# Kernel tuning notes

Hardware: AMD Instinct MI355X
Metric: run time of the kernel (lower is better)

## Reference

```python
import jax, jax.numpy as jnp
import numpy as np

# Assumptions (helpers not included in source):
#  - drop_edge(A, 0.8, training) is identity at inference (training=False); we
#    implement the deterministic eval path.
#  - normalized_laplacian_tilde_matrix(A) = D~^{-1/2} (A + I) D~^{-1/2}, the
#    renormalization-trick adjacency (A_tilde = A + I, D~ = rowsum(A_tilde)).

def setup_inputs() -> dict:
    key = jax.random.key(0)
    kx, kA, kW = jax.random.split(key, 3)
    B, C, Co, T, N, K = 64, 64, 64, 32, 64, 3
    x = jax.random.normal(kx, (B, C, T, N), dtype=jnp.float32)
    A = jax.random.uniform(kA, (B, K, T, N, N), dtype=jnp.float32)
    W = jax.random.normal(kW, (Co, C), dtype=jnp.float32) * 0.02  # 1x1 conv weight
    b = jnp.zeros((Co,), dtype=jnp.float32)
    return {"x": x, "A": A, "W": W, "b": b}


def reference(x, A, W, b):
    # 1x1 Conv2d == per-position channel mixing
    x = jnp.einsum('bctn,oc->botn', x, W) + b[None, :, None, None]

    # Vectorized normalized-Laplacian-tilde over all (B, K, T) graphs at once.
    N = A.shape[-1]
    A_tilde = A + jnp.eye(N, dtype=A.dtype)            # (B,K,T,N,N)
    deg = jnp.sum(A_tilde, axis=-1)                    # (B,K,T,N)
    dinv = jax.lax.rsqrt(deg)                          # deg >= 1, safe
    A_norm = A_tilde * dinv[..., :, None] * dinv[..., None, :]

    # Per-(k,t) bmm: out[b,c,t,m] = sum_k sum_n x[b,c,t,n] * A_norm[b,k,t,n,m]
    x_out = jnp.einsum('bctn,bktnm->bctm', x, A_norm)
    return (x_out, A)
```

## Files before the change

kernel.cpp:

```cpp
#include <hip/hip_runtime.h>
#include <hip/hip_bf16.h>

typedef __attribute__((ext_vector_type(8))) short short8;
typedef __attribute__((ext_vector_type(4))) short short4v;
typedef __attribute__((ext_vector_type(4))) float f32x4;

#define Bb 64
#define Cc 64
#define Tt 32
#define Nn 64
#define Kk 3
#define PITCH 72
#define OUT_A_OFF 8388608L

__device__ __forceinline__ short f2bf(float f) {
    __hip_bfloat16 h = __float2bfloat16(f);
    return *reinterpret_cast<short*>(&h);
}

__global__ __launch_bounds__(256, 4) void ctg_kernel(
    const float* __restrict__ X,
    const float* __restrict__ A,
    const float* __restrict__ W,
    const float* __restrict__ bias,
    float* __restrict__ out)
{
    __shared__ short sW [Cc * PITCH];
    __shared__ short sXT[Nn * PITCH];
    __shared__ short sX1[Cc * PITCH];
    __shared__ short sAT[Nn * PITCH];
    __shared__ float sDinv[Nn];
    __shared__ float sB[Cc];

    const int tid = threadIdx.x;
    const int b = blockIdx.x >> 5;
    const int t = blockIdx.x & 31;
    const int l  = tid & 63;
    const int w  = tid >> 6;
    const int lr = l & 15;
    const int lq = l >> 4;

    const long xbase = (long)b * (Cc * Tt * Nn) + (long)t * Nn;

    #pragma unroll
    for (int j = 0; j < 4; ++j) {
        int q  = tid + 256 * j;
        int r  = q >> 4;
        int c0 = (q & 15) * 4;
        f32x4 wv = *(const f32x4*)(W + r * 64 + c0);
        short4v ws;
        #pragma unroll
        for (int i = 0; i < 4; ++i) ws[i] = f2bf(wv[i]);
        *(short4v*)&sW[r * PITCH + c0] = ws;
        f32x4 xv = *(const f32x4*)(X + xbase + (long)r * (Tt * Nn) + c0);
        #pragma unroll
        for (int i = 0; i < 4; ++i) sXT[(c0 + i) * PITCH + r] = f2bf(xv[i]);
    }
    if (tid < Cc) sB[tid] = bias[tid];
    __syncthreads();

    short8 aw0 = *(const short8*)&sW[(16 * w + lr) * PITCH + 8 * lq];
    short8 aw1 = *(const short8*)&sW[(16 * w + lr) * PITCH + 32 + 8 * lq];
    f32x4 acc1[4];
    #pragma unroll
    for (int nt = 0; nt < 4; ++nt) {
        acc1[nt] = (f32x4){0.f, 0.f, 0.f, 0.f};
        short8 b0 = *(const short8*)&sXT[(16 * nt + lr) * PITCH + 8 * lq];
        short8 b1 = *(const short8*)&sXT[(16 * nt + lr) * PITCH + 32 + 8 * lq];
        acc1[nt] = __builtin_amdgcn_mfma_f32_16x16x32_bf16(aw0, b0, acc1[nt], 0, 0, 0);
        acc1[nt] = __builtin_amdgcn_mfma_f32_16x16x32_bf16(aw1, b1, acc1[nt], 0, 0, 0);
    }
    #pragma unroll
    for (int nt = 0; nt < 4; ++nt)
        #pragma unroll
        for (int r = 0; r < 4; ++r) {
            int c = 16 * w + 4 * lq + r;
            sX1[c * PITCH + 16 * nt + lr] = f2bf(acc1[nt][r] + sB[c]);
        }

    f32x4 acc3[4];
    #pragma unroll
    for (int mt = 0; mt < 4; ++mt) acc3[mt] = (f32x4){0.f, 0.f, 0.f, 0.f};

    const int m0 = (tid & 15) * 4;
    const long Abase0 = (long)b * (Kk * Tt * Nn * Nn) + (long)t * (Nn * Nn);

    for (int k = 0; k < Kk; ++k) {
        __syncthreads();

        const long Ab = Abase0 + (long)k * (Tt * Nn * Nn);
        f32x4 av[4];
        #pragma unroll
        for (int e = 0; e < 4; ++e) av[e] = *(const f32x4*)(A + Ab + 4 * (tid + 256 * e));
        #pragma unroll
        for (int e = 0; e < 4; ++e) *(f32x4*)(out + OUT_A_OFF + Ab + 4 * (tid + 256 * e)) = av[e];

        float dg[4];
        #pragma unroll
        for (int e = 0; e < 4; ++e) {
            float q = av[e][0] + av[e][1] + av[e][2] + av[e][3];
            q += __shfl_xor(q, 1);
            q += __shfl_xor(q, 2);
            q += __shfl_xor(q, 4);
            q += __shfl_xor(q, 8);
            dg[e] = q;
        }
        if ((tid & 15) == 0) {
            #pragma unroll
            for (int e = 0; e < 4; ++e)
                sDinv[(tid >> 4) + 16 * e] = rsqrtf(dg[e] + 1.0f);
        }
        __syncthreads();

        float dm[4] = { sDinv[m0], sDinv[m0 + 1], sDinv[m0 + 2], sDinv[m0 + 3] };
        #pragma unroll
        for (int e = 0; e < 4; ++e) {
            int n = (tid >> 4) + 16 * e;
            float dn = sDinv[n];
            #pragma unroll
            for (int i = 0; i < 4; ++i) {
                float v = av[e][i];
                if (m0 + i == n) v += 1.0f;
                sAT[(m0 + i) * PITCH + n] = f2bf(v * dn * dm[i]);
            }
        }
        __syncthreads();

        short8 a0 = *(const short8*)&sX1[(16 * w + lr) * PITCH + 8 * lq];
        short8 a1 = *(const short8*)&sX1[(16 * w + lr) * PITCH + 32 + 8 * lq];
        #pragma unroll
        for (int mt = 0; mt < 4; ++mt) {
            short8 b0 = *(const short8*)&sAT[(16 * mt + lr) * PITCH + 8 * lq];
            short8 b1 = *(const short8*)&sAT[(16 * mt + lr) * PITCH + 32 + 8 * lq];
            acc3[mt] = __builtin_amdgcn_mfma_f32_16x16x32_bf16(a0, b0, acc3[mt], 0, 0, 0);
            acc3[mt] = __builtin_amdgcn_mfma_f32_16x16x32_bf16(a1, b1, acc3[mt], 0, 0, 0);
        }
    }

    #pragma unroll
    for (int mt = 0; mt < 4; ++mt)
        #pragma unroll
        for (int r = 0; r < 4; ++r) {
            int c = 16 * w + 4 * lq + r;
            out[xbase + (long)c * (Tt * Nn) + 16 * mt + lr] = acc3[mt][r];
        }
}

extern "C" void kernel_launch(void* const* d_in, const int* in_sizes, int n_in,
                              void* d_out, int out_size, void* d_ws, size_t ws_size,
                              hipStream_t stream) {
    const float* X    = (const float*)d_in[0];
    const float* A    = (const float*)d_in[1];
    const float* W    = (const float*)d_in[2];
    const float* bias = (const float*)d_in[3];
    float* out = (float*)d_out;
    ctg_kernel<<<dim3(Bb * Tt), dim3(256), 0, stream>>>(X, A, W, bias, out);
}
```

Measured before the change: 243.6 us.

## Sum normalized adjacency over K in registers before a single MFMA pass

The kernel now builds the normalized adjacency for each k in registers and sums it over K in fp32. It then writes the summed matrix to shared memory once and runs one MFMA pass, instead of staging and multiplying per k. This removes two block barriers per k and two-thirds of the shared-memory staging and MFMA work for the graph product. It also adds an XOR-swizzled 64-wide shared layout and loads W and bias directly into registers. Occupancy is raised via launch bounds (256, 8), and outputs use nontemporal stores. The costs are more live registers for the 4x4 accumulators and different rounding, since the bf16 conversion now happens after the K-sum.

```diff
diff --git a/kernel.cpp b/kernel.cpp
--- a/kernel.cpp
+++ b/kernel.cpp
@@ -2,7 +2,6 @@
 #include <hip/hip_bf16.h>
 
 typedef __attribute__((ext_vector_type(8))) short short8;
-typedef __attribute__((ext_vector_type(4))) short short4v;
 typedef __attribute__((ext_vector_type(4))) float f32x4;
 
 #define Bb 64
@@ -18,55 +17,67 @@
     return *reinterpret_cast<short*>(&h);
 }
 
-__global__ __launch_bounds__(256, 4) void ctg_kernel(
+#define SWZ(row) ((((row) >> 3) ^ (row)) & 7)
+#define SADDR(row, col) (((row) << 6) + ((col) ^ (SWZ(row) << 3)))
+
+__global__ __launch_bounds__(256, 8) void ctg_kernel(
     const float* __restrict__ X,
     const float* __restrict__ A,
     const float* __restrict__ W,
     const float* __restrict__ bias,
     float* __restrict__ out)
 {
-    __shared__ short sW [Cc * PITCH];
-    __shared__ short sXT[Nn * PITCH];
-    __shared__ short sX1[Cc * PITCH];
-    __shared__ short sAT[Nn * PITCH];
-    __shared__ float sDinv[Nn];
-    __shared__ float sB[Cc];
+    __shared__ __attribute__((aligned(16))) short sU [64 * 64];
+    __shared__ __attribute__((aligned(16))) short sX1[Cc * PITCH];
+    __shared__ __attribute__((aligned(16))) float sDv[Kk][Nn];
 
-    const int tid = threadIdx.x;
-    const int b = blockIdx.x >> 5;
-    const int t = blockIdx.x & 31;
-    const int l  = tid & 63;
-    const int w  = tid >> 6;
-    const int lr = l & 15;
-    const int lq = l >> 4;
+    const int tid  = threadIdx.x;
+    const int b    = blockIdx.x >> 5;
+    const int t    = blockIdx.x & 31;
+    const int l    = tid & 63;
+    const int w    = tid >> 6;
+    const int lr   = l & 15;
+    const int lq   = l >> 4;
+    const int m0   = 4 * (tid & 15);
+    const int nrow = tid >> 4;
 
-    const long xbase = (long)b * (Cc * Tt * Nn) + (long)t * Nn;
+    const long xbase  = (long)b * (Cc * Tt * Nn) + (long)t * Nn;
+    const long Abase0 = (long)b * (Kk * Tt * Nn * Nn) + (long)t * (Nn * Nn);
 
     #pragma unroll
     for (int j = 0; j < 4; ++j) {
-        int q  = tid + 256 * j;
-        int r  = q >> 4;
-        int c0 = (q & 15) * 4;
-        f32x4 wv = *(const f32x4*)(W + r * 64 + c0);
-        short4v ws;
+        int c  = nrow + 16 * j;
+        f32x4 xv = *(const f32x4*)(X + xbase + (long)c * (Tt * Nn) + m0);
         #pragma unroll
-        for (int i = 0; i < 4; ++i) ws[i] = f2bf(wv[i]);
-        *(short4v*)&sW[r * PITCH + c0] = ws;
-        f32x4 xv = *(const f32x4*)(X + xbase + (long)r * (Tt * Nn) + c0);
-        #pragma unroll
-        for (int i = 0; i < 4; ++i) sXT[(c0 + i) * PITCH + r] = f2bf(xv[i]);
+        for (int i = 0; i < 4; ++i)
+            sU[SADDR(m0 + i, c)] = f2bf(xv[i]);
     }
-    if (tid < Cc) sB[tid] = bias[tid];
+
+    const float* wrow = W + (16 * w + lr) * Cc;
+    f32x4 wv0 = *(const f32x4*)(wrow + 8 * lq);
+    f32x4 wv1 = *(const f32x4*)(wrow + 8 * lq + 4);
+    f32x4 wv2 = *(const f32x4*)(wrow + 32 + 8 * lq);
+    f32x4 wv3 = *(const f32x4*)(wrow + 32 + 8 * lq + 4);
+    f32x4 bv  = *(const f32x4*)(bias + 16 * w + 4 * lq);
+    short8 aw0, aw1;
+    #pragma unroll
+    for (int i = 0; i < 4; ++i) {
+        aw0[i]     = f2bf(wv0[i]);
+        aw0[i + 4] = f2bf(wv1[i]);
+        aw1[i]     = f2bf(wv2[i]);
+        aw1[i + 4] = f2bf(wv3[i]);
+    }
+
     __syncthreads();
 
-    short8 aw0 = *(const short8*)&sW[(16 * w + lr) * PITCH + 8 * lq];
-    short8 aw1 = *(const short8*)&sW[(16 * w + lr) * PITCH + 32 + 8 * lq];
     f32x4 acc1[4];
     #pragma unroll
     for (int nt = 0; nt < 4; ++nt) {
+        const int row = 16 * nt + lr;
+        const int sw  = SWZ(row);
+        short8 b0 = *(const short8*)&sU[(row << 6) + ((lq ^ sw) << 3)];
+        short8 b1 = *(const short8*)&sU[(row << 6) + (((4 + lq) ^ sw) << 3)];
         acc1[nt] = (f32x4){0.f, 0.f, 0.f, 0.f};
-        short8 b0 = *(const short8*)&sXT[(16 * nt + lr) * PITCH + 8 * lq];
-        short8 b1 = *(const short8*)&sXT[(16 * nt + lr) * PITCH + 32 + 8 * lq];
         acc1[nt] = __builtin_amdgcn_mfma_f32_16x16x32_bf16(aw0, b0, acc1[nt], 0, 0, 0);
         acc1[nt] = __builtin_amdgcn_mfma_f32_16x16x32_bf16(aw1, b1, acc1[nt], 0, 0, 0);
     }
@@ -75,27 +86,26 @@
         #pragma unroll
         for (int r = 0; r < 4; ++r) {
             int c = 16 * w + 4 * lq + r;
-            sX1[c * PITCH + 16 * nt + lr] = f2bf(acc1[nt][r] + sB[c]);
+            sX1[c * PITCH + 16 * nt + lr] = f2bf(acc1[nt][r] + bv[r]);
         }
 
-    f32x4 acc3[4];
+    float S[4][4];
     #pragma unroll
-    for (int mt = 0; mt < 4; ++mt) acc3[mt] = (f32x4){0.f, 0.f, 0.f, 0.f};
-
-    const int m0 = (tid & 15) * 4;
-    const long Abase0 = (long)b * (Kk * Tt * Nn * Nn) + (long)t * (Nn * Nn);
+    for (int e = 0; e < 4; ++e)
+        #pragma unroll
+        for (int i = 0; i < 4; ++i) S[e][i] = 0.f;
 
     for (int k = 0; k < Kk; ++k) {
-        __syncthreads();
-
         const long Ab = Abase0 + (long)k * (Tt * Nn * Nn);
         f32x4 av[4];
         #pragma unroll
-        for (int e = 0; e < 4; ++e) av[e] = *(const f32x4*)(A + Ab + 4 * (tid + 256 * e));
+        for (int e = 0; e < 4; ++e)
+            av[e] = *(const f32x4*)(A + Ab + 4 * (tid + 256 * e));
         #pragma unroll
-        for (int e = 0; e < 4; ++e) *(f32x4*)(out + OUT_A_OFF + Ab + 4 * (tid + 256 * e)) = av[e];
+        for (int e = 0; e < 4; ++e)
+            __builtin_nontemporal_store(av[e], (f32x4*)(out + OUT_A_OFF + Ab + 4 * (tid + 256 * e)));
 
-        float dg[4];
+        float dnv[4];
         #pragma unroll
         for (int e = 0; e < 4; ++e) {
             float q = av[e][0] + av[e][1] + av[e][2] + av[e][3];
@@ -103,38 +113,49 @@
             q += __shfl_xor(q, 2);
             q += __shfl_xor(q, 4);
             q += __shfl_xor(q, 8);
-            dg[e] = q;
+            dnv[e] = rsqrtf(q + 1.0f);
         }
         if ((tid & 15) == 0) {
             #pragma unroll
-            for (int e = 0; e < 4; ++e)
-                sDinv[(tid >> 4) + 16 * e] = rsqrtf(dg[e] + 1.0f);
+            for (int e = 0; e < 4; ++e) sDv[k][nrow + 16 * e] = dnv[e];
         }
         __syncthreads();
 
-        float dm[4] = { sDinv[m0], sDinv[m0 + 1], sDinv[m0 + 2], sDinv[m0 + 3] };
+        f32x4 dm = *(const f32x4*)&sDv[k][m0];
         #pragma unroll
         for (int e = 0; e < 4; ++e) {
-            int n = (tid >> 4) + 16 * e;
-            float dn = sDinv[n];
+            const int n  = nrow + 16 * e;
+            const float dn = dnv[e];
             #pragma unroll
             for (int i = 0; i < 4; ++i) {
                 float v = av[e][i];
                 if (m0 + i == n) v += 1.0f;
-                sAT[(m0 + i) * PITCH + n] = f2bf(v * dn * dm[i]);
+                S[e][i] += v * dn * dm[i];
             }
         }
-        __syncthreads();
+    }
 
-        short8 a0 = *(const short8*)&sX1[(16 * w + lr) * PITCH + 8 * lq];
-        short8 a1 = *(const short8*)&sX1[(16 * w + lr) * PITCH + 32 + 8 * lq];
+    #pragma unroll
+    for (int e = 0; e < 4; ++e) {
+        int n = nrow + 16 * e;
         #pragma unroll
-        for (int mt = 0; mt < 4; ++mt) {
-            short8 b0 = *(const short8*)&sAT[(16 * mt + lr) * PITCH + 8 * lq];
-            short8 b1 = *(const short8*)&sAT[(16 * mt + lr) * PITCH + 32 + 8 * lq];
-            acc3[mt] = __builtin_amdgcn_mfma_f32_16x16x32_bf16(a0, b0, acc3[mt], 0, 0, 0);
-            acc3[mt] = __builtin_amdgcn_mfma_f32_16x16x32_bf16(a1, b1, acc3[mt], 0, 0, 0);
-        }
+        for (int i = 0; i < 4; ++i)
+            sU[SADDR(m0 + i, n)] = f2bf(S[e][i]);
+    }
+    __syncthreads();
+
+    const short8 a0 = *(const short8*)&sX1[(16 * w + lr) * PITCH + 8 * lq];
+    const short8 a1 = *(const short8*)&sX1[(16 * w + lr) * PITCH + 32 + 8 * lq];
+    f32x4 acc3[4];
+    #pragma unroll
+    for (int mt = 0; mt < 4; ++mt) {
+        const int row = 16 * mt + lr;
+        const int sw  = SWZ(row);
+        short8 b0 = *(const short8*)&sU[(row << 6) + ((lq ^ sw) << 3)];
+        short8 b1 = *(const short8*)&sU[(row << 6) + (((4 + lq) ^ sw) << 3)];
+        acc3[mt] = (f32x4){0.f, 0.f, 0.f, 0.f};
+        acc3[mt] = __builtin_amdgcn_mfma_f32_16x16x32_bf16(a0, b0, acc3[mt], 0, 0, 0);
+        acc3[mt] = __builtin_amdgcn_mfma_f32_16x16x32_bf16(a1, b1, acc3[mt], 0, 0, 0);
     }
 
     #pragma unroll
@@ -142,7 +163,8 @@
         #pragma unroll
         for (int r = 0; r < 4; ++r) {
             int c = 16 * w + 4 * lq + r;
-            out[xbase + (long)c * (Tt * Nn) + 16 * mt + lr] = acc3[mt][r];
+            __builtin_nontemporal_store(acc3[mt][r],
+                out + xbase + (long)c * (Tt * Nn) + 16 * mt + lr);
         }
 }
 
```

Result: slower. 288.7 us (+18.5%).
